# Performance work log

Measured on AMD Instinct MI355X. Metric: run time of the kernel, lower is better.

Reference implementation:

```python
import jax, jax.numpy as jnp
import numpy as np

B, D, H, C = 8192, 384, 256, 6
K_MIN, K_MAX = 4, 16
LN_EPS = 1e-5


def setup_inputs() -> dict:
    key = jax.random.key(0)
    ks = jax.random.split(key, 6)
    s = lambda k, shape: (jax.random.normal(k, shape, jnp.float32) * 0.05)
    return {
        "x": jax.random.normal(ks[0], (B, D), jnp.float32),
        "W_proj": s(ks[1], (D, H)), "b_proj": jnp.zeros((H,), jnp.float32),
        "W_tau": s(ks[2], (D, 1)), "b_tau": jnp.zeros((1,), jnp.float32),
        "W_res": s(ks[3], (H, H)), "b_res": jnp.zeros((H,), jnp.float32),
        "ln_g": jnp.ones((H,), jnp.float32), "ln_b": jnp.zeros((H,), jnp.float32),
        "W_fc": s(ks[4], (H, C)), "b_fc": jnp.zeros((C,), jnp.float32),
    }


def reference(x, W_proj, b_proj, W_tau, b_tau, W_res, b_res, ln_g, ln_b, W_fc, b_fc):
    # adaptive k per sample (torch path casts to int -> non-differentiable)
    tau = jax.nn.sigmoid(x @ W_tau + b_tau)[:, 0]                      # [B]
    k = jax.lax.stop_gradient(
        jnp.clip(jnp.round(K_MAX - (K_MAX - K_MIN) * tau), 1, K_MAX)
    ).astype(jnp.int32)                                                # [B]

    # pairwise squared distances (same nearest-neighbor ordering as cdist)
    sq = jnp.sum(x * x, axis=-1)                                       # [B]
    d2 = sq[:, None] + sq[None, :] - 2.0 * (x @ x.T)                   # [B,B]
    _, idx = jax.lax.top_k(-jax.lax.stop_gradient(d2), K_MAX)          # [B,K_MAX] nearest (incl. self)

    h = jax.nn.relu(x @ W_proj + b_proj)                               # [B,H]

    # ragged top-k mean via fixed K_MAX gather + position mask
    gathered = h[idx]                                                  # [B,K_MAX,H]
    mask = (jnp.arange(K_MAX)[None, :] < k[:, None]).astype(h.dtype)   # [B,K_MAX]
    agg = jnp.einsum('bkh,bk->bh', gathered, mask) / k[:, None].astype(h.dtype)

    r = jax.nn.relu(agg @ W_res + b_res)                               # [B,H]
    z = h + r
    mu = jnp.mean(z, axis=-1, keepdims=True)
    var = jnp.var(z, axis=-1, keepdims=True)
    zn = (z - mu) / jnp.sqrt(var + LN_EPS)
    return (zn * ln_g + ln_b) @ W_fc + b_fc                            # [B,C]
```

## Files before the change

kernel.cpp:

```cpp
#include <hip/hip_runtime.h>
#include <hip/hip_fp16.h>
#include <math.h>

#define NROWS 8192
#define DDIM 384
#define HDIM 256
#define CDIM 6
#define LN_EPS 1e-5f
#define DSTR 138
#define NTILES ((NROWS/128) * (NROWS/128 + 1) / 2)
#define NGEMM1 ((NROWS/128) * (HDIM/128))

typedef short bf16x8 __attribute__((ext_vector_type(8)));
typedef float f32x4 __attribute__((ext_vector_type(4)));
typedef unsigned short u16x8 __attribute__((ext_vector_type(8)));
typedef unsigned short u16x4 __attribute__((ext_vector_type(4)));
typedef unsigned short u16x2 __attribute__((ext_vector_type(2)));

__device__ __forceinline__ bool dj_better(float d1, int j1, float d2, int j2) {
    return (d1 < d2) || (d1 == d2 && j1 < j2);
}

__device__ __forceinline__ unsigned int umin_(unsigned int a, unsigned int b) { return a < b ? a : b; }
__device__ __forceinline__ unsigned int umax_(unsigned int a, unsigned int b) { return a > b ? a : b; }

__device__ __forceinline__ unsigned short map16f(float v) {
    union { _Float16 f; unsigned short u; } c;
    c.f = (_Float16)v;
    unsigned short b = c.u;
    return (unsigned short)(b ^ (unsigned short)((((short)b) >> 15) | 0x8000));
}

__device__ __forceinline__ float unmap16(unsigned int m16b) {
    unsigned short fb = (m16b & 0x8000u) ? (unsigned short)(m16b ^ 0x8000u)
                                         : (unsigned short)(~m16b);
    union { unsigned short u; _Float16 f; } cv; cv.u = fb;
    return (float)cv.f;
}

__device__ __forceinline__ unsigned short rne_bf16(float v) {
    unsigned int u = __float_as_uint(v);
    u += 0x7fffu + ((u >> 16) & 1u);
    return (unsigned short)(u >> 16);
}

__device__ __forceinline__ void ins8(
    unsigned int& s0, unsigned int& s1, unsigned int& s2, unsigned int& s3,
    unsigned int& s4, unsigned int& s5, unsigned int& s6, unsigned int& s7,
    unsigned int& m, unsigned int key)
{
    if (key < m) {
        s0 = (s0 == m) ? key : s0;
        s1 = (s1 == m) ? key : s1;
        s2 = (s2 == m) ? key : s2;
        s3 = (s3 == m) ? key : s3;
        s4 = (s4 == m) ? key : s4;
        s5 = (s5 == m) ? key : s5;
        s6 = (s6 == m) ? key : s6;
        s7 = (s7 == m) ? key : s7;
        m = umax_(umax_(umax_(s0, s1), umax_(s2, s3)),
                  umax_(umax_(s4, s5), umax_(s6, s7)));
    }
}

__device__ __forceinline__ unsigned int max8_(
    unsigned int s0, unsigned int s1, unsigned int s2, unsigned int s3,
    unsigned int s4, unsigned int s5, unsigned int s6, unsigned int s7)
{
    return umax_(umax_(umax_(s0, s1), umax_(s2, s3)),
                 umax_(umax_(s4, s5), umax_(s6, s7)));
}

__device__ __forceinline__ void sins8(
    unsigned int& s0, unsigned int& s1, unsigned int& s2, unsigned int& s3,
    unsigned int& s4, unsigned int& s5, unsigned int& s6, unsigned int& s7,
    unsigned int key)
{
    unsigned int t = umin_(s0, key);
    s0 = umax_(t, s1); t = umin_(t, s1);
    s1 = umax_(t, s2); t = umin_(t, s2);
    s2 = umax_(t, s3); t = umin_(t, s3);
    s3 = umax_(t, s4); t = umin_(t, s4);
    s4 = umax_(t, s5); t = umin_(t, s5);
    s5 = umax_(t, s6); t = umin_(t, s6);
    s6 = umax_(t, s7); s7 = umin_(t, s7);
}

#define CE_(a, b) { unsigned int hi_ = umax_(a, b), lo_ = umin_(a, b); a = hi_; b = lo_; }
#define SORT8_DESC(s0, s1, s2, s3, s4, s5, s6, s7) \
    CE_(s0, s1) CE_(s2, s3) CE_(s4, s5) CE_(s6, s7) \
    CE_(s0, s2) CE_(s1, s3) CE_(s4, s6) CE_(s5, s7) \
    CE_(s1, s2) CE_(s5, s6) CE_(s0, s4) CE_(s3, s7) \
    CE_(s1, s5) CE_(s2, s6) \
    CE_(s1, s4) CE_(s3, s6) \
    CE_(s2, s4) CE_(s3, s5) \
    CE_(s3, s4)

__global__ void __launch_bounds__(256) prep_kernel(
    const float* __restrict__ x, const float* __restrict__ W_tau,
    const float* __restrict__ b_tau, unsigned short* __restrict__ xb,
    float* __restrict__ sq, int* __restrict__ kk,
    const float* __restrict__ Wp, unsigned short* __restrict__ wpT,
    const float* __restrict__ Wr, unsigned short* __restrict__ wrT)
{
    int tid = threadIdx.x;
    if (blockIdx.x < NROWS / 4) {
        int wave = tid >> 6, lane = tid & 63;
        int row = blockIdx.x * 4 + wave;
        const float* xr = x + (size_t)row * DDIM;
        unsigned short* xbr = xb + (size_t)row * DDIM;
        float s = 0.f, tp = 0.f;
        #pragma unroll
        for (int q = 0; q < 6; ++q) {
            float v = xr[lane + 64 * q];
            xbr[lane + 64 * q] = rne_bf16(v);
            s = fmaf(v, v, s);
            tp = fmaf(v, W_tau[lane + 64 * q], tp);
        }
        #pragma unroll
        for (int off = 32; off > 0; off >>= 1) {
            s += __shfl_xor(s, off);
            tp += __shfl_xor(tp, off);
        }
        if (lane == 0) {
            sq[row] = s;
            float u = tp + b_tau[0];
            float tau = 1.f / (1.f + expf(-u));
            float kf = rintf(16.f - 12.f * tau);
            int k = (int)kf;
            k = min(16, max(1, k));
            kk[row] = k;
        }
    } else {
        int i = (blockIdx.x - NROWS / 4) * 256 + tid;
        if (i < DDIM * HDIM) {
            int k = i / HDIM, n = i % HDIM;
            wpT[(size_t)n * DDIM + k] = rne_bf16(Wp[i]);
        } else {
            int j = i - DDIM * HDIM;
            if (j < HDIM * HDIM) {
                int k = j / HDIM, n = j % HDIM;
                wrT[(size_t)n * HDIM + k] = rne_bf16(Wr[j]);
            }
        }
    }
}

__device__ __forceinline__ void gemm_kloop(
    const unsigned short* __restrict__ A, const unsigned short* __restrict__ B,
    const int K, const int rowbase, const int nbase,
    unsigned short* S, f32x4 (&acc)[4][4])
{
    const int tid = threadIdx.x;
    const int wave = tid >> 6;
    const int lane = tid & 63;
    const int wr = (wave >> 1) * 64;
    const int wc = (wave & 1) * 64;
    const int m16 = lane & 15;
    const int kq = lane >> 4;
    const int er0 = tid >> 2;
    const int er1 = 64 + (tid >> 2);
    const int eko = tid & 3;
    const int NK = K >> 5;

    auto stage = [&](int kb, int set) {
        const int k0 = kb * 32;
        char* Ad = (char*)S + set * 8192;
        char* Bd = (char*)S + 16384 + set * 8192;
        __builtin_amdgcn_global_load_lds(
            (const __attribute__((address_space(1))) void*)(A + (size_t)(rowbase + er0) * K + k0 + eko * 8),
            (__attribute__((address_space(3))) void*)(Ad + (wave * 64) * 16), 16, 0, 0);
        __builtin_amdgcn_global_load_lds(
            (const __attribute__((address_space(1))) void*)(A + (size_t)(rowbase + er1) * K + k0 + eko * 8),
            (__attribute__((address_space(3))) void*)(Ad + (256 + wave * 64) * 16), 16, 0, 0);
        __builtin_amdgcn_global_load_lds(
            (const __attribute__((address_space(1))) void*)(B + (size_t)(nbase + er0) * K + k0 + eko * 8),
            (__attribute__((address_space(3))) void*)(Bd + (wave * 64) * 16), 16, 0, 0);
        __builtin_amdgcn_global_load_lds(
            (const __attribute__((address_space(1))) void*)(B + (size_t)(nbase + er1) * K + k0 + eko * 8),
            (__attribute__((address_space(3))) void*)(Bd + (256 + wave * 64) * 16), 16, 0, 0);
    };

    stage(0, 0);
    __syncthreads();
    for (int kb = 0; kb < NK; ++kb) {
        const int cur = kb & 1;
        if (kb + 1 < NK) stage(kb + 1, cur ^ 1);
        const unsigned short* Ab = S + cur * 4096;
        const unsigned short* Bb = S + 8192 + cur * 4096;
        bf16x8 af[4], bfr[4];
        #pragma unroll
        for (int s = 0; s < 4; ++s) {
            af[s]  = *(const bf16x8*)&Ab[(wr + s * 16 + m16) * 32 + kq * 8];
            bfr[s] = *(const bf16x8*)&Bb[(wc + s * 16 + m16) * 32 + kq * 8];
        }
        #pragma unroll
        for (int si = 0; si < 4; ++si)
            #pragma unroll
            for (int sj = 0; sj < 4; ++sj)
                acc[si][sj] = __builtin_amdgcn_mfma_f32_16x16x32_bf16(
                    af[si], bfr[sj], acc[si][sj], 0, 0, 0);
        __syncthreads();
    }
}

__device__ __forceinline__ void gemm_epilogue(
    const float* __restrict__ bias, float* __restrict__ out,
    unsigned short* __restrict__ hb, const int rowbase, const int nbase,
    f32x4 (&acc)[4][4])
{
    const int lane = threadIdx.x & 63;
    const int wave = threadIdx.x >> 6;
    const int wr = (wave >> 1) * 64;
    const int wc = (wave & 1) * 64;
    const int m16 = lane & 15;
    const int kq = lane >> 4;
    #pragma unroll
    for (int sj = 0; sj < 4; ++sj) {
        int c = nbase + wc + sj * 16 + m16;
        float bc = bias[c];
        #pragma unroll
        for (int si = 0; si < 4; ++si) {
            int r = rowbase + wr + si * 16 + kq * 4;
            #pragma unroll
            for (int v = 0; v < 4; ++v) {
                float val = fmaxf(acc[si][sj][v] + bc, 0.f);
                out[(size_t)(r + v) * HDIM + c] = val;
                if (hb) hb[(size_t)(r + v) * HDIM + c] = rne_bf16(val);
            }
        }
    }
}

__global__ void __launch_bounds__(256) mfma_gemm_bias_relu_kernel(
    const unsigned short* __restrict__ A, const unsigned short* __restrict__ WT,
    const float* __restrict__ bias, float* __restrict__ out,
    unsigned short* __restrict__ hb, int K)
{
    __shared__ __align__(16) unsigned short S[16384];
    f32x4 acc[4][4];
    #pragma unroll
    for (int a = 0; a < 4; ++a)
        #pragma unroll
        for (int b = 0; b < 4; ++b)
            acc[a][b] = (f32x4){0.f, 0.f, 0.f, 0.f};
    gemm_kloop(A, WT, K, blockIdx.x * 128, blockIdx.y * 128, S, acc);
    gemm_epilogue(bias, out, hb, blockIdx.x * 128, blockIdx.y * 128, acc);
}

__global__ void __launch_bounds__(256) dist_gemm_fused_kernel(
    const unsigned short* __restrict__ xb, const float* __restrict__ sq,
    unsigned int* __restrict__ keys,
    const unsigned short* __restrict__ wpT, const float* __restrict__ b_proj,
    float* __restrict__ h, unsigned short* __restrict__ hb)
{
    __shared__ __align__(16) unsigned short SMEM[128 * DSTR];

    f32x4 acc[4][4];
    #pragma unroll
    for (int a = 0; a < 4; ++a)
        #pragma unroll
        for (int b = 0; b < 4; ++b)
            acc[a][b] = (f32x4){0.f, 0.f, 0.f, 0.f};

    if (blockIdx.x < NGEMM1) {
        const int rb = (blockIdx.x >> 1) * 128;
        const int nb = (blockIdx.x & 1) * 128;
        gemm_kloop(xb, wpT, DDIM, rb, nb, SMEM, acc);
        gemm_epilogue(b_proj, h, hb, rb, nb, acc);
        return;
    }

    int t = blockIdx.x - NGEMM1;
    int bi = (int)((sqrtf(8.f * (float)t + 1.f) - 1.f) * 0.5f);
    while ((bi + 1) * (bi + 2) / 2 <= t) ++bi;
    while (bi * (bi + 1) / 2 > t) --bi;
    int bj = t - bi * (bi + 1) / 2;

    const int tid = threadIdx.x;
    const int wave = tid >> 6;
    const int lane = tid & 63;
    const int rowbase = bi * 128;
    const int colbase = bj * 128;
    const int wr = (wave >> 1) * 64;
    const int wc = (wave & 1) * 64;
    const int m16 = lane & 15;
    const int kq = lane >> 4;

    gemm_kloop(xb, xb, DDIM, rowbase, colbase, SMEM, acc);
    unsigned short* Dt = SMEM;

    const int sr = tid >> 1;
    const int seg = tid & 1;

    {
        float sqc[4];
        #pragma unroll
        for (int sj = 0; sj < 4; ++sj) sqc[sj] = sq[colbase + wc + sj * 16 + m16];
        #pragma unroll
        for (int si = 0; si < 4; ++si)
            #pragma unroll
            for (int sj = 0; sj < 4; ++sj) {
                int r = wr + si * 16 + kq * 4;
                int c = wc + sj * 16 + m16;
                #pragma unroll
                for (int v = 0; v < 4; ++v)
                    Dt[(r + v) * DSTR + c] = map16f(sqc[sj] - 2.0f * acc[si][sj][v]);
            }
        __syncthreads();

        const unsigned short* rowp = &Dt[sr * DSTR + seg * 64];
        const int cb0 = colbase + seg * 64;
        u16x8 c0 = *(const u16x8*)rowp;
        unsigned int s0 = ((unsigned int)c0[0] << 13) | (unsigned int)(cb0 + 0);
        unsigned int s1 = ((unsigned int)c0[1] << 13) | (unsigned int)(cb0 + 1);
        unsigned int s2 = ((unsigned int)c0[2] << 13) | (unsigned int)(cb0 + 2);
        unsigned int s3 = ((unsigned int)c0[3] << 13) | (unsigned int)(cb0 + 3);
        unsigned int s4 = ((unsigned int)c0[4] << 13) | (unsigned int)(cb0 + 4);
        unsigned int s5 = ((unsigned int)c0[5] << 13) | (unsigned int)(cb0 + 5);
        unsigned int s6 = ((unsigned int)c0[6] << 13) | (unsigned int)(cb0 + 6);
        unsigned int s7 = ((unsigned int)c0[7] << 13) | (unsigned int)(cb0 + 7);
        SORT8_DESC(s0, s1, s2, s3, s4, s5, s6, s7);
        #pragma unroll
        for (int i = 1; i < 8; ++i) {
            u16x8 ch = *(const u16x8*)(rowp + i * 8);
            int cb = cb0 + i * 8;
            #pragma unroll
            for (int e = 0; e < 8; ++e)
                sins8(s0, s1, s2, s3, s4, s5, s6, s7,
                      ((unsigned int)ch[e] << 13) | (unsigned int)(cb + e));
        }
        size_t kb = (size_t)(rowbase + sr) * 1024 + (size_t)bj * 16 + seg * 8;
        uint4 o0; o0.x = s0; o0.y = s1; o0.z = s2; o0.w = s3;
        uint4 o1; o1.x = s4; o1.y = s5; o1.z = s6; o1.w = s7;
        *(uint4*)&keys[kb] = o0;
        *(uint4*)&keys[kb + 4] = o1;
    }

    if (bi != bj) {
        __syncthreads();
        #pragma unroll
        for (int si = 0; si < 4; ++si) {
            float4 sqr4 = *(const float4*)&sq[rowbase + wr + si * 16 + kq * 4];
            float srw[4] = {sqr4.x, sqr4.y, sqr4.z, sqr4.w};
            #pragma unroll
            for (int sj = 0; sj < 4; ++sj) {
                int r = wr + si * 16 + kq * 4;
                int c = wc + sj * 16 + m16;
                unsigned short h4[4];
                #pragma unroll
                for (int v = 0; v < 4; ++v)
                    h4[v] = map16f(srw[v] - 2.0f * acc[si][sj][v]);
                *(unsigned long long*)&Dt[c * DSTR + r] = *(unsigned long long*)h4;
            }
        }
        __syncthreads();

        const unsigned short* rowp = &Dt[sr * DSTR + seg * 64];
        const int cb0 = rowbase + seg * 64;
        u16x8 c0 = *(const u16x8*)rowp;
        unsigned int s0 = ((unsigned int)c0[0] << 13) | (unsigned int)(cb0 + 0);
        unsigned int s1 = ((unsigned int)c0[1] << 13) | (unsigned int)(cb0 + 1);
        unsigned int s2 = ((unsigned int)c0[2] << 13) | (unsigned int)(cb0 + 2);
        unsigned int s3 = ((unsigned int)c0[3] << 13) | (unsigned int)(cb0 + 3);
        unsigned int s4 = ((unsigned int)c0[4] << 13) | (unsigned int)(cb0 + 4);
        unsigned int s5 = ((unsigned int)c0[5] << 13) | (unsigned int)(cb0 + 5);
        unsigned int s6 = ((unsigned int)c0[6] << 13) | (unsigned int)(cb0 + 6);
        unsigned int s7 = ((unsigned int)c0[7] << 13) | (unsigned int)(cb0 + 7);
        SORT8_DESC(s0, s1, s2, s3, s4, s5, s6, s7);
        #pragma unroll
        for (int i = 1; i < 8; ++i) {
            u16x8 ch = *(const u16x8*)(rowp + i * 8);
            int cb = cb0 + i * 8;
            #pragma unroll
            for (int e = 0; e < 8; ++e)
                sins8(s0, s1, s2, s3, s4, s5, s6, s7,
                      ((unsigned int)ch[e] << 13) | (unsigned int)(cb + e));
        }
        size_t kb = (size_t)(colbase + sr) * 1024 + (size_t)bi * 16 + seg * 8;
        uint4 o0; o0.x = s0; o0.y = s1; o0.z = s2; o0.w = s3;
        uint4 o1; o1.x = s4; o1.y = s5; o1.z = s6; o1.w = s7;
        *(uint4*)&keys[kb] = o0;
        *(uint4*)&keys[kb + 4] = o1;
    }
}

__global__ void __launch_bounds__(256) topk_rescore_agg_kernel(
    const unsigned int* __restrict__ keys, const float* __restrict__ x,
    const float* __restrict__ sq, const int* __restrict__ kk,
    const unsigned short* __restrict__ hb, unsigned short* __restrict__ aggb)
{
    const int w = threadIdx.x >> 6;
    const int row = blockIdx.x * 4 + w;
    const int lane = threadIdx.x & 63;
    __shared__ int sidx[4][16];

    const uint4* kp = (const uint4*)(keys + (size_t)row * 1024 + lane * 16);
    uint4 v0 = kp[0], v1 = kp[1];
    unsigned int s0 = v0.x, s1 = v0.y, s2 = v0.z, s3 = v0.w;
    unsigned int s4 = v1.x, s5 = v1.y, s6 = v1.z, s7 = v1.w;
    unsigned int m = max8_(s0, s1, s2, s3, s4, s5, s6, s7);
    #pragma unroll
    for (int q = 2; q < 4; ++q) {
        uint4 v = kp[q];
        unsigned int gmin = umin_(umin_(v.x, v.y), umin_(v.z, v.w));
        if (gmin < m) {
            ins8(s0, s1, s2, s3, s4, s5, s6, s7, m, v.x);
            ins8(s0, s1, s2, s3, s4, s5, s6, s7, m, v.y);
            ins8(s0, s1, s2, s3, s4, s5, s6, s7, m, v.z);
            ins8(s0, s1, s2, s3, s4, s5, s6, s7, m, v.w);
        }
    }
    unsigned int lmin = umin_(umin_(umin_(s0, s1), umin_(s2, s3)),
                              umin_(umin_(s4, s5), umin_(s6, s7)));
    unsigned int myout = 0;
    for (int t = 0; t < 32; ++t) {
        unsigned int wv = lmin;
        #pragma unroll
        for (int off = 32; off > 0; off >>= 1)
            wv = umin_(wv, (unsigned int)__shfl_xor((int)wv, off));
        if (lane == t) myout = wv;
        if (lmin == wv) {
            s0 = (s0 == wv) ? 0xFFFFFFFFu : s0;
            s1 = (s1 == wv) ? 0xFFFFFFFFu : s1;
            s2 = (s2 == wv) ? 0xFFFFFFFFu : s2;
            s3 = (s3 == wv) ? 0xFFFFFFFFu : s3;
            s4 = (s4 == wv) ? 0xFFFFFFFFu : s4;
            s5 = (s5 == wv) ? 0xFFFFFFFFu : s5;
            s6 = (s6 == wv) ? 0xFFFFFFFFu : s6;
            s7 = (s7 == wv) ? 0xFFFFFFFFu : s7;
            lmin = umin_(umin_(umin_(s0, s1), umin_(s2, s3)),
                         umin_(umin_(s4, s5), umin_(s6, s7)));
        }
    }
    int myj = (int)(myout & 8191u);
    float dscr = (lane < 32) ? unmap16(myout >> 13) : INFINITY;

    const float EPS2 = 2.5f;
    const int k = kk[row];
    float d_k   = __shfl(dscr, k);
    float d_km1 = __shfl(dscr, k - 1);
    bool cin = false, amb = false;
    if (lane < 32) {
        if (lane < k) { cin = (dscr + EPS2 <= d_k); amb = !cin; }
        else          { amb = (dscr < d_km1 + EPS2); }
    }
    unsigned long long cinmask = __ballot(cin);
    unsigned long long ambmask = __ballot(amb);
    int n_in = __popcll(cinmask);
    int msel = k - n_in;

    float d_ex = 0.f;
    if (msel > 0) {
        float xr[6];
        #pragma unroll
        for (int q = 0; q < 6; ++q) xr[q] = x[(size_t)row * DDIM + lane + 64 * q];
        float sqrow = sq[row];
        unsigned long long mm = ambmask;
        while (mm) {
            int c = (int)(__ffsll(mm) - 1);
            mm &= mm - 1;
            int j = __shfl(myj, c);
            const float* xc = x + (size_t)j * DDIM;
            float p = 0.f;
            #pragma unroll
            for (int q = 0; q < 6; ++q) p = fmaf(xr[q], xc[lane + 64 * q], p);
            #pragma unroll
            for (int off = 32; off > 0; off >>= 1) p += __shfl_xor(p, off);
            float d = sqrow + sq[j] - 2.f * p;
            if (lane == c) d_ex = d;
        }
        int selrank = 0;
        unsigned long long mm2 = ambmask;
        while (mm2) {
            int u = (int)(__ffsll(mm2) - 1);
            mm2 &= mm2 - 1;
            float du = __shfl(d_ex, u);
            int ju = __shfl(myj, u);
            if (u != lane && dj_better(du, ju, d_ex, myj)) ++selrank;
        }
        if (amb && selrank < msel)
            sidx[w][n_in + selrank] = myj;
    }
    if (cin) {
        int pos = __popcll(cinmask & ((1ull << lane) - 1ull));
        sidx[w][pos] = myj;
    }
    __syncthreads();

    float a0 = 0.f, a1 = 0.f, a2 = 0.f, a3 = 0.f;
    for (int t = 0; t < k; ++t) {
        uint2 v = *(const uint2*)(hb + (size_t)sidx[w][t] * HDIM + lane * 4);
        a0 += __uint_as_float(v.x << 16);
        a1 += __uint_as_float(v.x & 0xFFFF0000u);
        a2 += __uint_as_float(v.y << 16);
        a3 += __uint_as_float(v.y & 0xFFFF0000u);
    }
    float inv = 1.f / (float)k;
    unsigned int b0 = rne_bf16(a0 * inv);
    unsigned int b1 = rne_bf16(a1 * inv);
    unsigned int b2 = rne_bf16(a2 * inv);
    unsigned int b3 = rne_bf16(a3 * inv);
    uint2 o; o.x = b0 | (b1 << 16); o.y = b2 | (b3 << 16);
    *(uint2*)(aggb + (size_t)row * HDIM + lane * 4) = o;
}

__global__ void __launch_bounds__(256) ln_fc_kernel(
    const float* __restrict__ h, const float* __restrict__ r,
    const float* __restrict__ g, const float* __restrict__ bb,
    const float* __restrict__ W_fc, const float* __restrict__ b_fc,
    float* __restrict__ out)
{
    const int row = blockIdx.x * 4 + (threadIdx.x >> 6);
    const int lane = threadIdx.x & 63;
    const float* hp = h + (size_t)row * HDIM;
    const float* rp = r + (size_t)row * HDIM;

    float z[4];
    #pragma unroll
    for (int q = 0; q < 4; ++q)
        z[q] = hp[lane + 64 * q] + rp[lane + 64 * q];

    float s = z[0] + z[1] + z[2] + z[3];
    float s2 = z[0]*z[0] + z[1]*z[1] + z[2]*z[2] + z[3]*z[3];
    #pragma unroll
    for (int off = 32; off > 0; off >>= 1) {
        s += __shfl_xor(s, off);
        s2 += __shfl_xor(s2, off);
    }
    float mu = s / 256.f;
    float rstd = rsqrtf(s2 / 256.f - mu * mu + LN_EPS);

    float p[6] = {0.f, 0.f, 0.f, 0.f, 0.f, 0.f};
    #pragma unroll
    for (int q = 0; q < 4; ++q) {
        int i = lane + 64 * q;
        float val = (z[q] - mu) * rstd * g[i] + bb[i];
        #pragma unroll
        for (int c = 0; c < 6; ++c)
            p[c] = fmaf(val, W_fc[i * 6 + c], p[c]);
    }
    #pragma unroll
    for (int c = 0; c < 6; ++c)
        #pragma unroll
        for (int off = 32; off > 0; off >>= 1) p[c] += __shfl_xor(p[c], off);

    if (lane < 6) {
        float o = p[0];
        o = (lane == 1) ? p[1] : o;
        o = (lane == 2) ? p[2] : o;
        o = (lane == 3) ? p[3] : o;
        o = (lane == 4) ? p[4] : o;
        o = (lane == 5) ? p[5] : o;
        out[(size_t)row * CDIM + lane] = o + b_fc[lane];
    }
}

extern "C" void kernel_launch(void* const* d_in, const int* in_sizes, int n_in,
                              void* d_out, int out_size, void* d_ws, size_t ws_size,
                              hipStream_t stream) {
    const float* x      = (const float*)d_in[0];
    const float* W_proj = (const float*)d_in[1];
    const float* b_proj = (const float*)d_in[2];
    const float* W_tau  = (const float*)d_in[3];
    const float* b_tau  = (const float*)d_in[4];
    const float* W_res  = (const float*)d_in[5];
    const float* b_res  = (const float*)d_in[6];
    const float* ln_g   = (const float*)d_in[7];
    const float* ln_b   = (const float*)d_in[8];
    const float* W_fc   = (const float*)d_in[9];
    const float* b_fc   = (const float*)d_in[10];
    float* out = (float*)d_out;

    char* ws = (char*)d_ws;
    float* sq   = (float*)ws;                        ws += (size_t)NROWS * 4;
    int*   kk   = (int*)ws;                          ws += (size_t)NROWS * 4;
    float* h    = (float*)ws;                        ws += (size_t)NROWS * HDIM * 4;
    float* r    = (float*)ws;                        ws += (size_t)NROWS * HDIM * 4;
    unsigned short* xb   = (unsigned short*)ws;      ws += (size_t)NROWS * DDIM * 2;
    unsigned short* hbuf = (unsigned short*)ws;      ws += (size_t)NROWS * HDIM * 2;
    unsigned short* aggb = (unsigned short*)ws;      ws += (size_t)NROWS * HDIM * 2;
    unsigned short* wpT  = (unsigned short*)ws;      ws += (size_t)DDIM * HDIM * 2;
    unsigned short* wrT  = (unsigned short*)ws;      ws += (size_t)HDIM * HDIM * 2;
    ws = (char*)(((size_t)ws + 255) & ~(size_t)255);
    unsigned int* keys = (unsigned int*)ws;          ws += (size_t)NROWS * 1024 * 4;

    const int prepW = (DDIM * HDIM + HDIM * HDIM + 255) / 256;
    prep_kernel<<<NROWS / 4 + prepW, 256, 0, stream>>>(
        x, W_tau, b_tau, xb, sq, kk, W_proj, wpT, W_res, wrT);
    dist_gemm_fused_kernel<<<NGEMM1 + NTILES, 256, 0, stream>>>(
        xb, sq, keys, wpT, b_proj, h, hbuf);
    topk_rescore_agg_kernel<<<NROWS / 4, 256, 0, stream>>>(keys, x, sq, kk, hbuf, aggb);
    mfma_gemm_bias_relu_kernel<<<dim3(NROWS / 128, HDIM / 128), 256, 0, stream>>>(
        aggb, wrT, b_res, r, (unsigned short*)nullptr, HDIM);
    ln_fc_kernel<<<NROWS / 4, 256, 0, stream>>>(h, r, ln_g, ln_b, W_fc, b_fc, out);
}
```

Before: 219.3 us.

## Process tile pairs per block, overlapping deferred transposed scan with next GEMM

Each distance block now handles two triangular tiles. The transposed-side top-8 scan of the first tile is deferred and interleaved, one chunk per k-step, with the global_load_lds staging and MFMA loop of the second tile, so scan ALU work overlaps memory and matrix work. The change also adds a separate LDS staging area, an inline k-loop using direct-to-LDS loads, a tile-order swizzle, and launch_bounds with 3 blocks per SU. Trade-offs are higher register and LDS pressure, half as many blocks for load balance, and extra synchronisation.

```diff
diff --git a/kernel.cpp b/kernel.cpp
--- a/kernel.cpp
+++ b/kernel.cpp
@@ -9,13 +9,12 @@
 #define LN_EPS 1e-5f
 #define DSTR 138
 #define NTILES ((NROWS/128) * (NROWS/128 + 1) / 2)
+#define NPAIRS (NTILES / 2)
 #define NGEMM1 ((NROWS/128) * (HDIM/128))
 
 typedef short bf16x8 __attribute__((ext_vector_type(8)));
 typedef float f32x4 __attribute__((ext_vector_type(4)));
 typedef unsigned short u16x8 __attribute__((ext_vector_type(8)));
-typedef unsigned short u16x4 __attribute__((ext_vector_type(4)));
-typedef unsigned short u16x2 __attribute__((ext_vector_type(2)));
 
 __device__ __forceinline__ bool dj_better(float d1, int j1, float d2, int j2) {
     return (d1 < d2) || (d1 == d2 && j1 < j2);
@@ -71,30 +70,61 @@
                  umax_(umax_(s4, s5), umax_(s6, s7)));
 }
 
-__device__ __forceinline__ void sins8(
-    unsigned int& s0, unsigned int& s1, unsigned int& s2, unsigned int& s3,
-    unsigned int& s4, unsigned int& s5, unsigned int& s6, unsigned int& s7,
-    unsigned int key)
-{
-    unsigned int t = umin_(s0, key);
-    s0 = umax_(t, s1); t = umin_(t, s1);
-    s1 = umax_(t, s2); t = umin_(t, s2);
-    s2 = umax_(t, s3); t = umin_(t, s3);
-    s3 = umax_(t, s4); t = umin_(t, s4);
-    s4 = umax_(t, s5); t = umin_(t, s5);
-    s5 = umax_(t, s6); t = umin_(t, s6);
-    s6 = umax_(t, s7); s7 = umin_(t, s7);
+__device__ __forceinline__ void sins8a(unsigned int (&s)[8], unsigned int key)
+{
+    unsigned int t = umin_(s[0], key);
+    s[0] = umax_(t, s[1]); t = umin_(t, s[1]);
+    s[1] = umax_(t, s[2]); t = umin_(t, s[2]);
+    s[2] = umax_(t, s[3]); t = umin_(t, s[3]);
+    s[3] = umax_(t, s[4]); t = umin_(t, s[4]);
+    s[4] = umax_(t, s[5]); t = umin_(t, s[5]);
+    s[5] = umax_(t, s[6]); t = umin_(t, s[6]);
+    s[6] = umax_(t, s[7]); s[7] = umin_(t, s[7]);
 }
 
 #define CE_(a, b) { unsigned int hi_ = umax_(a, b), lo_ = umin_(a, b); a = hi_; b = lo_; }
-#define SORT8_DESC(s0, s1, s2, s3, s4, s5, s6, s7) \
-    CE_(s0, s1) CE_(s2, s3) CE_(s4, s5) CE_(s6, s7) \
-    CE_(s0, s2) CE_(s1, s3) CE_(s4, s6) CE_(s5, s7) \
-    CE_(s1, s2) CE_(s5, s6) CE_(s0, s4) CE_(s3, s7) \
-    CE_(s1, s5) CE_(s2, s6) \
-    CE_(s1, s4) CE_(s3, s6) \
-    CE_(s2, s4) CE_(s3, s5) \
-    CE_(s3, s4)
+#define SORT8A_DESC(s) \
+    CE_(s[0], s[1]) CE_(s[2], s[3]) CE_(s[4], s[5]) CE_(s[6], s[7]) \
+    CE_(s[0], s[2]) CE_(s[1], s[3]) CE_(s[4], s[6]) CE_(s[5], s[7]) \
+    CE_(s[1], s[2]) CE_(s[5], s[6]) CE_(s[0], s[4]) CE_(s[3], s[7]) \
+    CE_(s[1], s[5]) CE_(s[2], s[6]) \
+    CE_(s[1], s[4]) CE_(s[3], s[6]) \
+    CE_(s[2], s[4]) CE_(s[3], s[5]) \
+    CE_(s[3], s[4])
+
+__device__ __forceinline__ void scan_seed(
+    const unsigned short* rowp, int cb0, unsigned int (&s)[8])
+{
+    u16x8 c0 = *(const u16x8*)rowp;
+    s[0] = ((unsigned int)c0[0] << 13) | (unsigned int)(cb0 + 0);
+    s[1] = ((unsigned int)c0[1] << 13) | (unsigned int)(cb0 + 1);
+    s[2] = ((unsigned int)c0[2] << 13) | (unsigned int)(cb0 + 2);
+    s[3] = ((unsigned int)c0[3] << 13) | (unsigned int)(cb0 + 3);
+    s[4] = ((unsigned int)c0[4] << 13) | (unsigned int)(cb0 + 4);
+    s[5] = ((unsigned int)c0[5] << 13) | (unsigned int)(cb0 + 5);
+    s[6] = ((unsigned int)c0[6] << 13) | (unsigned int)(cb0 + 6);
+    s[7] = ((unsigned int)c0[7] << 13) | (unsigned int)(cb0 + 7);
+    SORT8A_DESC(s)
+}
+
+__device__ __forceinline__ void scan_chunk_i(
+    const unsigned short* rowp, int cb0, int i, unsigned int (&s)[8])
+{
+    u16x8 ch = *(const u16x8*)(rowp + i * 8);
+    int cb = cb0 + i * 8;
+    #pragma unroll
+    for (int e = 0; e < 8; ++e)
+        sins8a(s, ((unsigned int)ch[e] << 13) | (unsigned int)(cb + e));
+}
+
+__device__ __forceinline__ void scan_emit(
+    const unsigned int (&s)[8], unsigned int* __restrict__ keys, size_t kb)
+{
+    uint4 o0; o0.x = s[0]; o0.y = s[1]; o0.z = s[2]; o0.w = s[3];
+    uint4 o1; o1.x = s[4]; o1.y = s[5]; o1.z = s[6]; o1.w = s[7];
+    *(uint4*)&keys[kb] = o0;
+    *(uint4*)&keys[kb + 4] = o1;
+}
 
 __global__ void __launch_bounds__(256) prep_kernel(
     const float* __restrict__ x, const float* __restrict__ W_tau,
@@ -248,22 +278,21 @@
     gemm_epilogue(bias, out, hb, blockIdx.x * 128, blockIdx.y * 128, acc);
 }
 
-__global__ void __launch_bounds__(256) dist_gemm_fused_kernel(
+__global__ void __launch_bounds__(256, 3) dist_gemm_fused_kernel(
     const unsigned short* __restrict__ xb, const float* __restrict__ sq,
     unsigned int* __restrict__ keys,
     const unsigned short* __restrict__ wpT, const float* __restrict__ b_proj,
     float* __restrict__ h, unsigned short* __restrict__ hb)
 {
-    __shared__ __align__(16) unsigned short SMEM[128 * DSTR];
-
-    f32x4 acc[4][4];
-    #pragma unroll
-    for (int a = 0; a < 4; ++a)
-        #pragma unroll
-        for (int b = 0; b < 4; ++b)
-            acc[a][b] = (f32x4){0.f, 0.f, 0.f, 0.f};
+    __shared__ __align__(16) unsigned short SMEM[128 * DSTR + 8192];
 
     if (blockIdx.x < NGEMM1) {
+        f32x4 acc[4][4];
+        #pragma unroll
+        for (int a = 0; a < 4; ++a)
+            #pragma unroll
+            for (int b = 0; b < 4; ++b)
+                acc[a][b] = (f32x4){0.f, 0.f, 0.f, 0.f};
         const int rb = (blockIdx.x >> 1) * 128;
         const int nb = (blockIdx.x & 1) * 128;
         gemm_kloop(xb, wpT, DDIM, rb, nb, SMEM, acc);
@@ -271,117 +300,149 @@
         return;
     }
 
-    int t = blockIdx.x - NGEMM1;
-    int bi = (int)((sqrtf(8.f * (float)t + 1.f) - 1.f) * 0.5f);
-    while ((bi + 1) * (bi + 2) / 2 <= t) ++bi;
-    while (bi * (bi + 1) / 2 > t) --bi;
-    int bj = t - bi * (bi + 1) / 2;
+    int p = blockIdx.x - NGEMM1;
+    p = (p & 7) * (NPAIRS / 8) + (p >> 3);
 
     const int tid = threadIdx.x;
     const int wave = tid >> 6;
     const int lane = tid & 63;
-    const int rowbase = bi * 128;
-    const int colbase = bj * 128;
     const int wr = (wave >> 1) * 64;
     const int wc = (wave & 1) * 64;
     const int m16 = lane & 15;
     const int kq = lane >> 4;
-
-    gemm_kloop(xb, xb, DDIM, rowbase, colbase, SMEM, acc);
-    unsigned short* Dt = SMEM;
-
+    const int er0 = tid >> 2;
+    const int er1 = 64 + (tid >> 2);
+    const int eko = tid & 3;
     const int sr = tid >> 1;
     const int seg = tid & 1;
 
-    {
-        float sqc[4];
-        #pragma unroll
-        for (int sj = 0; sj < 4; ++sj) sqc[sj] = sq[colbase + wc + sj * 16 + m16];
-        #pragma unroll
-        for (int si = 0; si < 4; ++si)
-            #pragma unroll
-            for (int sj = 0; sj < 4; ++sj) {
-                int r = wr + si * 16 + kq * 4;
-                int c = wc + sj * 16 + m16;
+    unsigned short* Dt = SMEM;
+    unsigned short* STG = SMEM + 128 * DSTR;
+    const unsigned short* rowp = &Dt[sr * DSTR + seg * 64];
+
+    bool have_def = false;
+    unsigned int dS[8];
+    int dcb0 = 0;
+    size_t dkb = 0;
+
+    for (int hf = 0; hf < 2; ++hf) {
+        int t = 2 * p + hf;
+        int bi = (int)((sqrtf(8.f * (float)t + 1.f) - 1.f) * 0.5f);
+        while ((bi + 1) * (bi + 2) / 2 <= t) ++bi;
+        while (bi * (bi + 1) / 2 > t) --bi;
+        int bj = t - bi * (bi + 1) / 2;
+        const int rowbase = bi * 128;
+        const int colbase = bj * 128;
+
+        f32x4 acc[4][4];
+        #pragma unroll
+        for (int a = 0; a < 4; ++a)
+            #pragma unroll
+            for (int b = 0; b < 4; ++b)
+                acc[a][b] = (f32x4){0.f, 0.f, 0.f, 0.f};
+
+        #pragma unroll
+        for (int kb = 0; kb < DDIM / 32; ++kb) {
+            const int k0 = kb * 32;
+            char* STb = (char*)STG;
+            __builtin_amdgcn_global_load_lds(
+                (const __attribute__((address_space(1))) void*)(xb + (size_t)(rowbase + er0) * DDIM + k0 + eko * 8),
+                (__attribute__((address_space(3))) void*)(STb + (wave * 64) * 16), 16, 0, 0);
+            __builtin_amdgcn_global_load_lds(
+                (const __attribute__((address_space(1))) void*)(xb + (size_t)(rowbase + er1) * DDIM + k0 + eko * 8),
+                (__attribute__((address_space(3))) void*)(STb + (256 + wave * 64) * 16), 16, 0, 0);
+            __builtin_amdgcn_global_load_lds(
+                (const __attribute__((address_space(1))) void*)(xb + (size_t)(colbase + er0) * DDIM + k0 + eko * 8),
+                (__attribute__((address_space(3))) void*)(STb + 8192 + (wave * 64) * 16), 16, 0, 0);
+            __builtin_amdgcn_global_load_lds(
+                (const __attribute__((address_space(1))) void*)(xb + (size_t)(colbase + er1) * DDIM + k0 + eko * 8),
+                (__attribute__((address_space(3))) void*)(STb + 8192 + (256 + wave * 64) * 16), 16, 0, 0);
+
+            if (have_def) {
+                if (kb == 0)      scan_seed(rowp, dcb0, dS);
+                else if (kb <= 7) scan_chunk_i(rowp, dcb0, kb, dS);
+            }
+            __syncthreads();
+
+            bf16x8 af[4], bfr[4];
+            #pragma unroll
+            for (int s = 0; s < 4; ++s) {
+                af[s]  = *(const bf16x8*)&STG[(wr + s * 16 + m16) * 32 + kq * 8];
+                bfr[s] = *(const bf16x8*)&STG[4096 + (wc + s * 16 + m16) * 32 + kq * 8];
+            }
+            #pragma unroll
+            for (int si = 0; si < 4; ++si)
                 #pragma unroll
-                for (int v = 0; v < 4; ++v)
-                    Dt[(r + v) * DSTR + c] = map16f(sqc[sj] - 2.0f * acc[si][sj][v]);
+                for (int sj = 0; sj < 4; ++sj)
+                    acc[si][sj] = __builtin_amdgcn_mfma_f32_16x16x32_bf16(
+                        af[si], bfr[sj], acc[si][sj], 0, 0, 0);
+            __syncthreads();
+        }
+        if (have_def) {
+            scan_emit(dS, keys, dkb);
+            have_def = false;
+        }
+
+        {
+            float sqc[4];
+            #pragma unroll
+            for (int sj = 0; sj < 4; ++sj) sqc[sj] = sq[colbase + wc + sj * 16 + m16];
+            #pragma unroll
+            for (int si = 0; si < 4; ++si)
+                #pragma unroll
+                for (int sj = 0; sj < 4; ++sj) {
+                    int r = wr + si * 16 + kq * 4;
+                    int c = wc + sj * 16 + m16;
+                    #pragma unroll
+                    for (int v = 0; v < 4; ++v)
+                        Dt[(r + v) * DSTR + c] = map16f(sqc[sj] - 2.0f * acc[si][sj][v]);
+                }
+            __syncthreads();
+
+            unsigned int S1[8];
+            scan_seed(rowp, colbase + seg * 64, S1);
+            #pragma unroll
+            for (int i = 1; i < 8; ++i)
+                scan_chunk_i(rowp, colbase + seg * 64, i, S1);
+            scan_emit(S1, keys,
+                      (size_t)(rowbase + sr) * 1024 + (size_t)bj * 16 + seg * 8);
+        }
+
+        if (bi != bj) {
+            __syncthreads();
+            #pragma unroll
+            for (int si = 0; si < 4; ++si) {
+                float4 sqr4 = *(const float4*)&sq[rowbase + wr + si * 16 + kq * 4];
+                float srw[4] = {sqr4.x, sqr4.y, sqr4.z, sqr4.w};
+                #pragma unroll
+                for (int sj = 0; sj < 4; ++sj) {
+                    int r = wr + si * 16 + kq * 4;
+                    int c = wc + sj * 16 + m16;
+                    unsigned short h4[4];
+                    #pragma unroll
+                    for (int v = 0; v < 4; ++v)
+                        h4[v] = map16f(srw[v] - 2.0f * acc[si][sj][v]);
+                    *(unsigned long long*)&Dt[c * DSTR + r] = *(unsigned long long*)h4;
+                }
             }
-        __syncthreads();
-
-        const unsigned short* rowp = &Dt[sr * DSTR + seg * 64];
-        const int cb0 = colbase + seg * 64;
-        u16x8 c0 = *(const u16x8*)rowp;
-        unsigned int s0 = ((unsigned int)c0[0] << 13) | (unsigned int)(cb0 + 0);
-        unsigned int s1 = ((unsigned int)c0[1] << 13) | (unsigned int)(cb0 + 1);
-        unsigned int s2 = ((unsigned int)c0[2] << 13) | (unsigned int)(cb0 + 2);
-        unsigned int s3 = ((unsigned int)c0[3] << 13) | (unsigned int)(cb0 + 3);
-        unsigned int s4 = ((unsigned int)c0[4] << 13) | (unsigned int)(cb0 + 4);
-        unsigned int s5 = ((unsigned int)c0[5] << 13) | (unsigned int)(cb0 + 5);
-        unsigned int s6 = ((unsigned int)c0[6] << 13) | (unsigned int)(cb0 + 6);
-        unsigned int s7 = ((unsigned int)c0[7] << 13) | (unsigned int)(cb0 + 7);
-        SORT8_DESC(s0, s1, s2, s3, s4, s5, s6, s7);
-        #pragma unroll
-        for (int i = 1; i < 8; ++i) {
-            u16x8 ch = *(const u16x8*)(rowp + i * 8);
-            int cb = cb0 + i * 8;
-            #pragma unroll
-            for (int e = 0; e < 8; ++e)
-                sins8(s0, s1, s2, s3, s4, s5, s6, s7,
-                      ((unsigned int)ch[e] << 13) | (unsigned int)(cb + e));
-        }
-        size_t kb = (size_t)(rowbase + sr) * 1024 + (size_t)bj * 16 + seg * 8;
-        uint4 o0; o0.x = s0; o0.y = s1; o0.z = s2; o0.w = s3;
-        uint4 o1; o1.x = s4; o1.y = s5; o1.z = s6; o1.w = s7;
-        *(uint4*)&keys[kb] = o0;
-        *(uint4*)&keys[kb + 4] = o1;
-    }
-
-    if (bi != bj) {
-        __syncthreads();
-        #pragma unroll
-        for (int si = 0; si < 4; ++si) {
-            float4 sqr4 = *(const float4*)&sq[rowbase + wr + si * 16 + kq * 4];
-            float srw[4] = {sqr4.x, sqr4.y, sqr4.z, sqr4.w};
-            #pragma unroll
-            for (int sj = 0; sj < 4; ++sj) {
-                int r = wr + si * 16 + kq * 4;
-                int c = wc + sj * 16 + m16;
-                unsigned short h4[4];
+            __syncthreads();
+
+            if (hf == 0) {
+                have_def = true;
+                dcb0 = rowbase + seg * 64;
+                dkb = (size_t)(colbase + sr) * 1024 + (size_t)bi * 16 + seg * 8;
+            } else {
+                unsigned int S2[8];
+                scan_seed(rowp, rowbase + seg * 64, S2);
                 #pragma unroll
-                for (int v = 0; v < 4; ++v)
-                    h4[v] = map16f(srw[v] - 2.0f * acc[si][sj][v]);
-                *(unsigned long long*)&Dt[c * DSTR + r] = *(unsigned long long*)h4;
+                for (int i = 1; i < 8; ++i)
+                    scan_chunk_i(rowp, rowbase + seg * 64, i, S2);
+                scan_emit(S2, keys,
+                          (size_t)(colbase + sr) * 1024 + (size_t)bi * 16 + seg * 8);
             }
-        }
-        __syncthreads();
-
-        const unsigned short* rowp = &Dt[sr * DSTR + seg * 64];
-        const int cb0 = rowbase + seg * 64;
-        u16x8 c0 = *(const u16x8*)rowp;
-        unsigned int s0 = ((unsigned int)c0[0] << 13) | (unsigned int)(cb0 + 0);
-        unsigned int s1 = ((unsigned int)c0[1] << 13) | (unsigned int)(cb0 + 1);
-        unsigned int s2 = ((unsigned int)c0[2] << 13) | (unsigned int)(cb0 + 2);
-        unsigned int s3 = ((unsigned int)c0[3] << 13) | (unsigned int)(cb0 + 3);
-        unsigned int s4 = ((unsigned int)c0[4] << 13) | (unsigned int)(cb0 + 4);
-        unsigned int s5 = ((unsigned int)c0[5] << 13) | (unsigned int)(cb0 + 5);
-        unsigned int s6 = ((unsigned int)c0[6] << 13) | (unsigned int)(cb0 + 6);
-        unsigned int s7 = ((unsigned int)c0[7] << 13) | (unsigned int)(cb0 + 7);
-        SORT8_DESC(s0, s1, s2, s3, s4, s5, s6, s7);
-        #pragma unroll
-        for (int i = 1; i < 8; ++i) {
-            u16x8 ch = *(const u16x8*)(rowp + i * 8);
-            int cb = cb0 + i * 8;
-            #pragma unroll
-            for (int e = 0; e < 8; ++e)
-                sins8(s0, s1, s2, s3, s4, s5, s6, s7,
-                      ((unsigned int)ch[e] << 13) | (unsigned int)(cb + e));
-        }
-        size_t kb = (size_t)(colbase + sr) * 1024 + (size_t)bi * 16 + seg * 8;
-        uint4 o0; o0.x = s0; o0.y = s1; o0.z = s2; o0.w = s3;
-        uint4 o1; o1.x = s4; o1.y = s5; o1.z = s6; o1.w = s7;
-        *(uint4*)&keys[kb] = o0;
-        *(uint4*)&keys[kb + 4] = o1;
+        } else if (hf == 0) {
+            __syncthreads();
+        }
     }
 }
 
@@ -588,7 +649,7 @@
     const int prepW = (DDIM * HDIM + HDIM * HDIM + 255) / 256;
     prep_kernel<<<NROWS / 4 + prepW, 256, 0, stream>>>(
         x, W_tau, b_tau, xb, sq, kk, W_proj, wpT, W_res, wrT);
-    dist_gemm_fused_kernel<<<NGEMM1 + NTILES, 256, 0, stream>>>(
+    dist_gemm_fused_kernel<<<NGEMM1 + NPAIRS, 256, 0, stream>>>(
         xb, sq, keys, wpT, b_proj, h, hbuf);
     topk_rescore_agg_kernel<<<NROWS / 4, 256, 0, stream>>>(keys, x, sq, kk, hbuf, aggb);
     mfma_gemm_bias_relu_kernel<<<dim3(NROWS / 128, HDIM / 128), 256, 0, stream>>>(
```

Result: slower. 228.0 us (+4.0%).
